# Performance work log

Hardware: AMD Instinct MI355X
Metric: run time of the kernel (lower is better)

The kernel has to match this reference:

```python
import jax, jax.numpy as jnp
import numpy as np

BETA = 0.9            # ensemble leak
FREQ_BETA = 0.95      # RunningAverage beta
TARGET_FREQ = 0.2
THRESH_UP = 0.05
THRESH_DOWN = 1.05

SHAPE = (128, 128)
S = SHAPE[0] * SHAPE[1]


def setup_inputs() -> dict:
    key = jax.random.key(0)
    k1, k2, k3, k4, k5 = jax.random.split(key, 5)
    x = jax.random.normal(k1, SHAPE, dtype=jnp.float32)
    activation = jax.random.normal(k2, SHAPE, dtype=jnp.float32)
    threshold = jnp.ones(SHAPE, dtype=jnp.float32)  # base_threshold = 1.0
    freq_activation = jax.random.uniform(k3, SHAPE, dtype=jnp.float32)
    # small-scale lateral weights so lateral input doesn't blow up
    lateral_weights = jax.random.normal(k4, (S, S), dtype=jnp.float32) * 0.01
    spikes = jax.random.randint(k5, SHAPE, 0, 2).astype(jnp.bool_)
    return {
        "x": x,
        "activation": activation,
        "threshold": threshold,
        "freq_activation": freq_activation,
        "lateral_weights": lateral_weights,
        "spikes": spikes,
    }


def reference(x, activation, threshold, freq_activation, lateral_weights, spikes):
    shape = x.shape
    # lateral_weights[spikes.view(-1), :].sum(dim=0) == spikes_float @ lateral_weights
    spikes_f = spikes.reshape(-1).astype(x.dtype)
    lateral_input = (spikes_f @ lateral_weights).reshape(shape)
    x_tot = x + lateral_input
    # leaky integration
    new_activation = BETA * activation + x_tot
    new_spikes = new_activation > threshold
    # auto gain control: running average of spike frequency
    new_freq = FREQ_BETA * freq_activation + (1.0 - FREQ_BETA) * new_spikes.astype(x.dtype)
    new_threshold = jnp.where(
        new_freq > TARGET_FREQ,
        threshold + THRESH_UP,
        jnp.where(new_freq < TARGET_FREQ, threshold / THRESH_DOWN, threshold),
    )
    # reset mechanism 'zero': zero out activation at spiking neurons
    new_activation = jnp.where(new_spikes, jnp.zeros((), x.dtype), new_activation)
    return new_spikes, new_activation, new_threshold, new_freq
```

## Files before the change

kernel.cpp:

```cpp
#include <hip/hip_runtime.h>
#include <hip/hip_bf16.h>
#include <stdint.h>


constexpr int S = 16384;
constexpr int TPB = 256;
constexpr int RPC = 64;
constexpr int N_CHUNKS = S / RPC;
constexpr int COL_BLOCKS = 4;
constexpr int COLW = S / COL_BLOCKS;

typedef float  f32x4 __attribute__((ext_vector_type(4)));
typedef double f64x4 __attribute__((ext_vector_type(4)));

__device__ __forceinline__ bool spike_flag(const void* sp, int c, int r) {
  if (c == 0) return ((const int*)sp)[r] != 0;
  if (c == 1) return ((const unsigned char*)sp)[r] != 0;
  if (c == 2) return ((const float*)sp)[r] != 0.0f;
  return ((const unsigned short*)sp)[r] != 0;
}

__device__ __forceinline__ int classify_local(const uint32_t* spw, int tid,
                                              int* sh3) {
  int l3a = 0, l3o = 0, lnz = 0;
  for (int w = tid; w < S / 4; w += TPB) {
    uint32_t v = spw[w];
#pragma unroll
    for (int b = 0; b < 4; ++b) {
      unsigned char byte = (v >> (8 * b)) & 0xFF;
      int i = w * 4 + b;
      if (byte == 0x3F) { l3a = 1; if ((i & 3) == 1) l3o = 1; }
      if (byte != 0 && (i & 3) != 0) lnz = 1;
    }
  }
  if (l3a) atomicOr(&sh3[0], 1);
  if (l3o) atomicOr(&sh3[1], 1);
  if (lnz) atomicOr(&sh3[2], 1);
  __syncthreads();
  return sh3[0] ? (sh3[1] ? 3 : 2) : (sh3[2] ? 1 : 0);
}

__global__ __launch_bounds__(TPB) void lateral_selfprep(
    const float* __restrict__ W, const void* __restrict__ sp,
    float* __restrict__ partial) {
  __shared__ int sh3[3];
  __shared__ int ids[RPC];
  __shared__ int n_s;
  const int tid = threadIdx.x;
  if (tid < 3) sh3[tid] = 0;
  __syncthreads();
  const int c = classify_local((const uint32_t*)sp, tid, sh3);

  const int b = blockIdx.y;
  const int q = blockIdx.x;
  if (tid < 64) {
    int r = b * RPC + tid;
    bool f = spike_flag(sp, c, r);
    unsigned long long m = __ballot(f);
    int within = __popcll(m & ((1ULL << tid) - 1ULL));
    if (f) ids[within] = r;
    if (tid == 0) n_s = __popcll(m);
  }
  __syncthreads();
  const int n = n_s;

  const float* Wc = W + q * COLW + tid * 4;
  f64x4 a0 = 0.0, a1 = 0.0, a2 = 0.0, a3 = 0.0;
  int i = 0;
  for (; i + 2 <= n; i += 2) {
    const float* pa = Wc + (size_t)ids[i] * S;
    const float* pb = Wc + (size_t)ids[i + 1] * S;
    f32x4 wa0 = __builtin_nontemporal_load((const f32x4*)(pa));
    f32x4 wa1 = __builtin_nontemporal_load((const f32x4*)(pa + 1024));
    f32x4 wa2 = __builtin_nontemporal_load((const f32x4*)(pa + 2048));
    f32x4 wa3 = __builtin_nontemporal_load((const f32x4*)(pa + 3072));
    f32x4 wb0 = __builtin_nontemporal_load((const f32x4*)(pb));
    f32x4 wb1 = __builtin_nontemporal_load((const f32x4*)(pb + 1024));
    f32x4 wb2 = __builtin_nontemporal_load((const f32x4*)(pb + 2048));
    f32x4 wb3 = __builtin_nontemporal_load((const f32x4*)(pb + 3072));
    a0 += __builtin_convertvector(wa0, f64x4) + __builtin_convertvector(wb0, f64x4);
    a1 += __builtin_convertvector(wa1, f64x4) + __builtin_convertvector(wb1, f64x4);
    a2 += __builtin_convertvector(wa2, f64x4) + __builtin_convertvector(wb2, f64x4);
    a3 += __builtin_convertvector(wa3, f64x4) + __builtin_convertvector(wb3, f64x4);
  }
  if (i < n) {
    const float* pa = Wc + (size_t)ids[i] * S;
    a0 += __builtin_convertvector(__builtin_nontemporal_load((const f32x4*)(pa)), f64x4);
    a1 += __builtin_convertvector(__builtin_nontemporal_load((const f32x4*)(pa + 1024)), f64x4);
    a2 += __builtin_convertvector(__builtin_nontemporal_load((const f32x4*)(pa + 2048)), f64x4);
    a3 += __builtin_convertvector(__builtin_nontemporal_load((const f32x4*)(pa + 3072)), f64x4);
  }
  float* dst = partial + (size_t)b * S + q * COLW + tid * 4;
  *(f32x4*)(dst)        = __builtin_convertvector(a0, f32x4);
  *(f32x4*)(dst + 1024) = __builtin_convertvector(a1, f32x4);
  *(f32x4*)(dst + 2048) = __builtin_convertvector(a2, f32x4);
  *(f32x4*)(dst + 3072) = __builtin_convertvector(a3, f32x4);
}

__device__ __forceinline__ void ensemble_epilogue(
    int j, float lateral,
    const float* __restrict__ x, const float* __restrict__ act,
    const float* __restrict__ thr, const float* __restrict__ freq,
    float* __restrict__ out) {
  float na = 0.9f * act[j] + x[j] + lateral;
  float t = thr[j];
  bool sp = na > t;
  float nf = 0.95f * freq[j] + 0.05f * (sp ? 1.0f : 0.0f);
  float nt = (nf > 0.2f) ? (t + 0.05f) : ((nf < 0.2f) ? (t / 1.05f) : t);
  if (sp) na = 0.0f;
  out[j]         = sp ? 1.0f : 0.0f;
  out[S + j]     = na;
  out[2 * S + j] = nt;
  out[3 * S + j] = nf;
}

__global__ __launch_bounds__(TPB) void ensemble_update(
    const float* __restrict__ partial,
    const float* __restrict__ x, const float* __restrict__ act,
    const float* __restrict__ thr, const float* __restrict__ freq,
    float* __restrict__ out) {
  const int j = blockIdx.x * TPB + threadIdx.x;
  double l0 = 0.0, l1 = 0.0, l2 = 0.0, l3 = 0.0;
#pragma unroll 8
  for (int c = 0; c < N_CHUNKS; c += 4) {
    l0 += (double)partial[(size_t)c * S + j];
    l1 += (double)partial[(size_t)(c + 1) * S + j];
    l2 += (double)partial[(size_t)(c + 2) * S + j];
    l3 += (double)partial[(size_t)(c + 3) * S + j];
  }
  ensemble_epilogue(j, (float)((l0 + l1) + (l2 + l3)), x, act, thr, freq, out);
}

__global__ __launch_bounds__(TPB) void fused_full_int(
    const float* __restrict__ W, const int* __restrict__ spikes,
    const float* __restrict__ x, const float* __restrict__ act,
    const float* __restrict__ thr, const float* __restrict__ freq,
    float* __restrict__ out) {
  const int j = blockIdx.x * TPB + threadIdx.x;
  double lat = 0.0;
  for (int i = 0; i < S; ++i)
    if (spikes[i] != 0) lat += (double)W[(size_t)i * S + j];
  ensemble_epilogue(j, (float)lat, x, act, thr, freq, out);
}

extern "C" void kernel_launch(void* const* d_in, const int* in_sizes, int n_in,
                              void* d_out, int out_size, void* d_ws, size_t ws_size,
                              hipStream_t stream) {
  const float* x    = (const float*)d_in[0];
  const float* act  = (const float*)d_in[1];
  const float* thr  = (const float*)d_in[2];
  const float* freq = (const float*)d_in[3];
  const float* W    = (const float*)d_in[4];
  const void*  sp   = d_in[5];
  float* out = (float*)d_out;

  const size_t need = (size_t)N_CHUNKS * S * sizeof(float);

  if (ws_size >= need) {
    float* partial = (float*)d_ws;
    dim3 g1(COL_BLOCKS, N_CHUNKS);
    lateral_selfprep<<<g1, TPB, 0, stream>>>(W, sp, partial);
    ensemble_update<<<S / TPB, TPB, 0, stream>>>(partial, x, act, thr, freq, out);
  } else {
    fused_full_int<<<S / TPB, TPB, 0, stream>>>(W, (const int*)sp, x, act, thr, freq, out);
  }
}
```

Before: 105.2 us.

## Replace partial-sum buffer with fixed-point 64-bit atomic accumulation

Each lateral block now converts its per-column double sums to 2^44-scaled fixed-point integers and atomically adds them into a single S-length 64-bit accumulator, replacing the 256xS partial-sum buffer. The finalize kernel reads one value per column instead of reducing 256 partials. This removes about 16 MB of partial writes and reads, at the cost of a memset launch and roughly 4M global 64-bit atomics that contend per column. Integer addition keeps the result deterministic.

```diff
diff --git a/kernel.cpp b/kernel.cpp
--- a/kernel.cpp
+++ b/kernel.cpp
@@ -9,6 +9,8 @@
 constexpr int N_CHUNKS = S / RPC;
 constexpr int COL_BLOCKS = 4;
 constexpr int COLW = S / COL_BLOCKS;
+
+constexpr double FP_SCALE = 17592186044416.0;
 
 typedef float  f32x4 __attribute__((ext_vector_type(4)));
 typedef double f64x4 __attribute__((ext_vector_type(4)));
@@ -40,9 +42,18 @@
   return sh3[0] ? (sh3[1] ? 3 : 2) : (sh3[2] ? 1 : 0);
 }
 
+__device__ __forceinline__ void atomic_acc4(unsigned long long* acc, int col,
+                                            f64x4 v) {
+#pragma unroll
+  for (int k = 0; k < 4; ++k) {
+    long long d = (long long)llrint(v[k] * FP_SCALE);
+    atomicAdd(acc + col + k, (unsigned long long)d);
+  }
+}
+
 __global__ __launch_bounds__(TPB) void lateral_selfprep(
     const float* __restrict__ W, const void* __restrict__ sp,
-    float* __restrict__ partial) {
+    unsigned long long* __restrict__ acc) {
   __shared__ int sh3[3];
   __shared__ int ids[RPC];
   __shared__ int n_s;
@@ -90,11 +101,11 @@
     a2 += __builtin_convertvector(__builtin_nontemporal_load((const f32x4*)(pa + 2048)), f64x4);
     a3 += __builtin_convertvector(__builtin_nontemporal_load((const f32x4*)(pa + 3072)), f64x4);
   }
-  float* dst = partial + (size_t)b * S + q * COLW + tid * 4;
-  *(f32x4*)(dst)        = __builtin_convertvector(a0, f32x4);
-  *(f32x4*)(dst + 1024) = __builtin_convertvector(a1, f32x4);
-  *(f32x4*)(dst + 2048) = __builtin_convertvector(a2, f32x4);
-  *(f32x4*)(dst + 3072) = __builtin_convertvector(a3, f32x4);
+  const int col0 = q * COLW + tid * 4;
+  atomic_acc4(acc, col0, a0);
+  atomic_acc4(acc, col0 + 1024, a1);
+  atomic_acc4(acc, col0 + 2048, a2);
+  atomic_acc4(acc, col0 + 3072, a3);
 }
 
 __device__ __forceinline__ void ensemble_epilogue(
@@ -115,20 +126,13 @@
 }
 
 __global__ __launch_bounds__(TPB) void ensemble_update(
-    const float* __restrict__ partial,
+    const unsigned long long* __restrict__ acc,
     const float* __restrict__ x, const float* __restrict__ act,
     const float* __restrict__ thr, const float* __restrict__ freq,
     float* __restrict__ out) {
   const int j = blockIdx.x * TPB + threadIdx.x;
-  double l0 = 0.0, l1 = 0.0, l2 = 0.0, l3 = 0.0;
-#pragma unroll 8
-  for (int c = 0; c < N_CHUNKS; c += 4) {
-    l0 += (double)partial[(size_t)c * S + j];
-    l1 += (double)partial[(size_t)(c + 1) * S + j];
-    l2 += (double)partial[(size_t)(c + 2) * S + j];
-    l3 += (double)partial[(size_t)(c + 3) * S + j];
-  }
-  ensemble_epilogue(j, (float)((l0 + l1) + (l2 + l3)), x, act, thr, freq, out);
+  double lat = (double)(long long)acc[j] / FP_SCALE;
+  ensemble_epilogue(j, (float)lat, x, act, thr, freq, out);
 }
 
 __global__ __launch_bounds__(TPB) void fused_full_int(
@@ -154,13 +158,14 @@
   const void*  sp   = d_in[5];
   float* out = (float*)d_out;
 
-  const size_t need = (size_t)N_CHUNKS * S * sizeof(float);
+  const size_t need = (size_t)S * sizeof(unsigned long long);
 
   if (ws_size >= need) {
-    float* partial = (float*)d_ws;
+    unsigned long long* acc = (unsigned long long*)d_ws;
+    hipMemsetAsync(acc, 0, need, stream);
     dim3 g1(COL_BLOCKS, N_CHUNKS);
-    lateral_selfprep<<<g1, TPB, 0, stream>>>(W, sp, partial);
-    ensemble_update<<<S / TPB, TPB, 0, stream>>>(partial, x, act, thr, freq, out);
+    lateral_selfprep<<<g1, TPB, 0, stream>>>(W, sp, acc);
+    ensemble_update<<<S / TPB, TPB, 0, stream>>>(acc, x, act, thr, freq, out);
   } else {
     fused_full_int<<<S / TPB, TPB, 0, stream>>>(W, (const int*)sp, x, act, thr, freq, out);
   }
```

After: 149.5 us. 1.42x slower.
